# Kernel tuning notes

Measured on AMD Instinct MI355X. Metric: run time of the kernel, lower is better.

Reference implementation:

```python
import jax, jax.numpy as jnp
import numpy as np

B, S, C, D, H, FF, DEPTH, T, N = 8, 1024, 2, 512, 8, 2048, 6, 64, 16
HD = D // H
EPS = 1e-5


def _ln(x, w, b):
    m = jnp.mean(x, axis=-1, keepdims=True)
    v = jnp.mean(jnp.square(x - m), axis=-1, keepdims=True)
    return (x - m) * jax.lax.rsqrt(v + EPS) * w + b


def setup_inputs() -> dict:
    key = jax.random.key(0)
    ks = jax.random.split(key, 24)
    w = lambda k, shape: (jax.random.normal(k, shape, jnp.float32) * 0.02)
    return {
        "src": jax.random.normal(ks[0], (B, S, D), jnp.float32),
        "ctx_emb": jax.random.normal(ks[1], (B, C, D), jnp.float32),
        "times": jax.random.randint(ks[2], (B, S), 0, T),
        "spaces": jax.random.randint(ks[3], (B, S), 0, N),
        "pad_mask": jnp.zeros((B, S + C), bool),
        "time_emb": w(ks[4], (T, D)),
        "space_emb": w(ks[5], (N, D)),
        "Wqkv": w(ks[6], (DEPTH, 3 * D, D)),
        "bqkv": jnp.zeros((DEPTH, 3 * D), jnp.float32),
        "Wo": w(ks[7], (DEPTH, D, D)),
        "bo": jnp.zeros((DEPTH, D), jnp.float32),
        "ln1_w": jnp.ones((DEPTH, D), jnp.float32),
        "ln1_b": jnp.zeros((DEPTH, D), jnp.float32),
        "W1": w(ks[8], (DEPTH, FF, D)),
        "b1": jnp.zeros((DEPTH, FF), jnp.float32),
        "W2": w(ks[9], (DEPTH, D, FF)),
        "b2": jnp.zeros((DEPTH, D), jnp.float32),
        "ln2_w": jnp.ones((DEPTH, D), jnp.float32),
        "ln2_b": jnp.zeros((DEPTH, D), jnp.float32),
    }


def _forward(src, ctx_emb, times, spaces, pad_mask, time_emb, space_emb,
             Wqkv, bqkv, Wo, bo, ln1_w, ln1_b, W1, b1, W2, b2, ln2_w, ln2_b):
    NEG = -jnp.inf
    # learned time/space positional embeddings, then append context tokens
    x = src + time_emb[times] + space_emb[spaces]          # [B,S,D]
    x = jnp.concatenate([x, ctx_emb], axis=1)              # [B,L,D], L=S+C
    # per-batch additive float mask: causal-in-time over src tokens,
    # ctx tokens attendable by everyone, ctx rows attend only to ctx.
    cond = times[:, :, None] >= times[:, None, :]          # [B,S,S]
    m = jnp.where(cond, 0.0, NEG)
    m = jnp.pad(m, ((0, 0), (0, C), (0, 0)), constant_values=NEG)  # ctx rows
    m = jnp.pad(m, ((0, 0), (0, 0), (0, C)), constant_values=0.0)  # ctx cols
    m = m + jnp.where(pad_mask[:, None, :], NEG, 0.0)      # key padding
    m = m[:, None]                                         # [B,1,L,L]

    scale = 1.0 / np.sqrt(HD)
    Bc, L, _ = x.shape
    for i in range(DEPTH):
        # --- self-attention (post-norm encoder layer) ---
        qkv = x @ Wqkv[i].T + bqkv[i]                      # [B,L,3D]
        q, k, v = jnp.split(qkv, 3, axis=-1)
        split = lambda t: t.reshape(Bc, L, H, HD).transpose(0, 2, 1, 3)
        q, k, v = split(q), split(k), split(v)             # [B,H,L,HD]
        scores = jnp.einsum('bhqd,bhkd->bhqk', q, k) * scale + m
        p = jax.nn.softmax(scores, axis=-1)
        a = jnp.einsum('bhqk,bhkd->bhqd', p, v)
        a = a.transpose(0, 2, 1, 3).reshape(Bc, L, D)
        a = a @ Wo[i].T + bo[i]
        x = _ln(x + a, ln1_w[i], ln1_b[i])
        # --- feed-forward ---
        h = jax.nn.gelu(x @ W1[i].T + b1[i], approximate=False)
        h = h @ W2[i].T + b2[i]
        x = _ln(x + h, ln2_w[i], ln2_b[i])
    return x[:, :S]                                        # drop ctx tokens


def reference(src, ctx_emb, times, spaces, pad_mask, time_emb, space_emb,
              Wqkv, bqkv, Wo, bo, ln1_w, ln1_b, W1, b1, W2, b2, ln2_w, ln2_b):
    return _forward(src, ctx_emb, times, spaces, pad_mask, time_emb, space_emb,
                    Wqkv, bqkv, Wo, bo, ln1_w, ln1_b, W1, b1, W2, b2, ln2_w, ln2_b)
```

## Files before the change

### kernel.cpp

```cpp
#include <hip/hip_runtime.h>
#include <hip/hip_bf16.h>

#define BB 8
#define SS 1024
#define CC 2
#define DD 512
#define NH 8
#define FF2 2048
#define NL 6
#define LL 1026
#define HD 64
#define MROWS 8208
#define MP 8320
#define KVPAD 1152

typedef __attribute__((ext_vector_type(8))) short bf16x8;
typedef __attribute__((ext_vector_type(4))) float f32x4;

typedef __attribute__((address_space(3))) void lds_void;
typedef __attribute__((address_space(1))) void g_void;

__device__ __forceinline__ void gll16(const void* g, void* l) {
  __builtin_amdgcn_global_load_lds((const g_void*)g, (lds_void*)l, 16, 0, 0);
}

__global__ __launch_bounds__(256) void cvt_bf16_k(const float* __restrict__ in,
                                                  __hip_bfloat16* __restrict__ out) {
  int i = (blockIdx.x * 256 + threadIdx.x) * 4;
  float4 v = *(const float4*)&in[i];
  out[i + 0] = __float2bfloat16(v.x);
  out[i + 1] = __float2bfloat16(v.y);
  out[i + 2] = __float2bfloat16(v.z);
  out[i + 3] = __float2bfloat16(v.w);
}

__global__ __launch_bounds__(256) void embed_k(const float* __restrict__ src,
    const float* __restrict__ ctx, const int* __restrict__ times,
    const int* __restrict__ spaces, const float* __restrict__ te,
    const float* __restrict__ se, float* __restrict__ x,
    __hip_bfloat16* __restrict__ xb) {
  int row = blockIdx.x;
  int b = row / LL, l = row % LL;
  int c = threadIdx.x * 2;
  float y0, y1;
  if (l < SS) {
    const float* sp = src + ((size_t)(b * SS + l)) * DD + c;
    int tt = times[b * SS + l], ssp = spaces[b * SS + l];
    y0 = sp[0] + te[tt * DD + c] + se[ssp * DD + c];
    y1 = sp[1] + te[tt * DD + c + 1] + se[ssp * DD + c + 1];
  } else {
    const float* cp = ctx + ((size_t)(b * CC + (l - SS))) * DD + c;
    y0 = cp[0]; y1 = cp[1];
  }
  size_t o = (size_t)row * DD + c;
  x[o] = y0; x[o + 1] = y1;
  xb[o] = __float2bfloat16(y0); xb[o + 1] = __float2bfloat16(y1);
}

template <int EPI>
__global__ __launch_bounds__(256) void gemm_bt(const __hip_bfloat16* __restrict__ A,
    const __hip_bfloat16* __restrict__ W, const float* __restrict__ bias,
    void* __restrict__ outp, int K, int N) {
  __shared__ __hip_bfloat16 As[128 * 64];
  __shared__ __hip_bfloat16 Bs[128 * 64];
  const int tid = threadIdx.x;
  const int lane = tid & 63, wv = tid >> 6;
  const int m0 = blockIdx.x * 128, n0 = blockIdx.y * 128;
  const int wr = wv >> 1, wc = wv & 1;
  const int r0 = lane & 15, kq = lane >> 4;
  f32x4 acc[4][4] = {};
  for (int k0 = 0; k0 < K; k0 += 64) {
    __syncthreads();
#pragma unroll
    for (int c = 0; c < 4; ++c) {
      int chb = c * 256 + wv * 64;
      int ch = chb + lane;
      int row = ch >> 3, cp = ch & 7;
      gll16(A + (size_t)(m0 + row) * K + k0 + cp * 8, (char*)As + chb * 16);
      gll16(W + (size_t)(n0 + row) * K + k0 + cp * 8, (char*)Bs + chb * 16);
    }
    __syncthreads();
#pragma unroll
    for (int kk = 0; kk < 64; kk += 32) {
      bf16x8 af[4], bfr[4];
#pragma unroll
      for (int m = 0; m < 4; ++m)
        af[m] = *(const bf16x8*)&As[(wr * 64 + m * 16 + r0) * 64 + kk + kq * 8];
#pragma unroll
      for (int n = 0; n < 4; ++n)
        bfr[n] = *(const bf16x8*)&Bs[(wc * 64 + n * 16 + r0) * 64 + kk + kq * 8];
#pragma unroll
      for (int m = 0; m < 4; ++m)
#pragma unroll
        for (int n = 0; n < 4; ++n)
          acc[m][n] = __builtin_amdgcn_mfma_f32_16x16x32_bf16(af[m], bfr[n], acc[m][n], 0, 0, 0);
    }
  }
#pragma unroll
  for (int m = 0; m < 4; ++m) {
    int grow_base = m0 + wr * 64 + m * 16 + kq * 4;
#pragma unroll
    for (int n = 0; n < 4; ++n) {
      int gcol = n0 + wc * 64 + n * 16 + r0;
      float bv = bias[gcol];
#pragma unroll
      for (int j = 0; j < 4; ++j) {
        int grow = grow_base + j;
        float v = acc[m][n][j] + bv;
        if (EPI == 2) v = 0.5f * v * (1.f + erff(v * 0.70710678f));
        if (EPI == 0)
          ((float*)outp)[(size_t)grow * N + gcol] = v;
        else
          ((__hip_bfloat16*)outp)[(size_t)grow * N + gcol] = __float2bfloat16(v);
      }
    }
  }
}

__global__ __launch_bounds__(256) void vtrans_k(const __hip_bfloat16* __restrict__ qkv,
                                                __hip_bfloat16* __restrict__ vt) {
  __shared__ __hip_bfloat16 tile[64][72];
  int bh = blockIdx.y;
  int b = bh >> 3, hh = bh & 7;
  int l0 = blockIdx.x * 64;
  int t = threadIdx.x;
  int lr = t >> 2, part = t & 3;
  int l = l0 + lr;
  if (l < LL) {
    const __hip_bfloat16* p = qkv + (size_t)(b * LL + l) * 1536 + 1024 + hh * 64 + part * 16;
    *(uint4*)&tile[lr][part * 16] = *(const uint4*)p;
    *(uint4*)&tile[lr][part * 16 + 8] = *(const uint4*)(p + 8);
  } else {
    uint4 z = make_uint4(0, 0, 0, 0);
    *(uint4*)&tile[lr][part * 16] = z;
    *(uint4*)&tile[lr][part * 16 + 8] = z;
  }
  __syncthreads();
  int d = t >> 2, kp = t & 3;
  __hip_bfloat16 vals[16];
#pragma unroll
  for (int i = 0; i < 16; ++i) vals[i] = tile[kp * 16 + i][d];
  __hip_bfloat16* o = vt + ((size_t)(bh * 64 + d)) * KVPAD + l0 + kp * 16;
  *(uint4*)o = *(uint4*)&vals[0];
  *(uint4*)(o + 8) = *(uint4*)&vals[8];
}

#define TK_CTX (-2000000000)
#define TQ_CTX (-1000000000)
#define TK_INV (2000000000)

__global__ __launch_bounds__(256) void attn_k(const __hip_bfloat16* __restrict__ qkv,
    const __hip_bfloat16* __restrict__ vt, const int* __restrict__ times,
    __hip_bfloat16* __restrict__ aout) {
  __shared__ __hip_bfloat16 Kl[128 * 64];
  __shared__ __hip_bfloat16 Vl[64 * 128];
  __shared__ __hip_bfloat16 Pl[4][16 * 128];
  const int tid = threadIdx.x, lane = tid & 63, wv = tid >> 6;
  const int r0 = lane & 15, kq = lane >> 4;
  int i = blockIdx.x;
  int xcd = i & 7, slot = i >> 3;
  int bhl = slot / 17;
  int qb = slot - bhl * 17;
  int bh = xcd * 8 + bhl;
  int b = bh >> 3, hh = bh & 7;
  char* plbase = (char*)&Pl[wv][0];

  const int qbase = qb * 64 + wv * 16;
  int qr = qbase + r0;
  if (qr > LL - 1) qr = LL - 1;
  const __hip_bfloat16* qp = qkv + (size_t)(b * LL + qr) * 1536 + hh * 64;
  bf16x8 qa0 = *(const bf16x8*)(qp + kq * 8);
  bf16x8 qa1 = *(const bf16x8*)(qp + 32 + kq * 8);
  int tq[4];
#pragma unroll
  for (int j = 0; j < 4; ++j) {
    int r = qbase + kq * 4 + j;
    tq[j] = (r < SS) ? times[b * SS + r] : TQ_CTX;
  }
  float m_run[4] = {-1e30f, -1e30f, -1e30f, -1e30f};
  float l_run[4] = {0.f, 0.f, 0.f, 0.f};
  f32x4 O[4] = {};
  const float scale = 0.125f;

  for (int kc = 0; kc < 9; ++kc) {
    __syncthreads();
#pragma unroll
    for (int c = 0; c < 4; ++c) {
      int chb = c * 256 + wv * 64;
      int ch = chb + lane;
      {
        int trow = ch >> 3, cp = ch & 7;
        int krow = kc * 128 + trow;
        if (krow > LL - 1) krow = LL - 1;
        int scp = cp ^ (trow & 7);
        gll16(qkv + (size_t)(b * LL + krow) * 1536 + 512 + hh * 64 + scp * 8,
              (char*)Kl + chb * 16);
      }
      {
        int d = ch >> 4, kp = ch & 15;
        int skp = kp ^ (d & 7);
        gll16(vt + ((size_t)(bh * 64 + d)) * KVPAD + kc * 128 + skp * 8,
              (char*)Vl + chb * 16);
      }
    }
    __syncthreads();
    f32x4 s[8] = {};
#pragma unroll
    for (int n = 0; n < 8; ++n) {
      int row = n * 16 + r0;
      bf16x8 kb0 = *(const bf16x8*)&Kl[row * 64 + ((kq ^ (row & 7)) * 8)];
      bf16x8 kb1 = *(const bf16x8*)&Kl[row * 64 + (((4 + kq) ^ (row & 7)) * 8)];
      s[n] = __builtin_amdgcn_mfma_f32_16x16x32_bf16(qa0, kb0, s[n], 0, 0, 0);
      s[n] = __builtin_amdgcn_mfma_f32_16x16x32_bf16(qa1, kb1, s[n], 0, 0, 0);
    }
    int tkn[8];
#pragma unroll
    for (int n = 0; n < 8; ++n) {
      int k = kc * 128 + 16 * n + r0;
      tkn[n] = (k < SS) ? times[b * SS + k] : ((k < LL) ? TK_CTX : TK_INV);
    }
    float mch[4] = {-1e30f, -1e30f, -1e30f, -1e30f};
#pragma unroll
    for (int n = 0; n < 8; ++n)
#pragma unroll
      for (int j = 0; j < 4; ++j) {
        float sv = (tq[j] >= tkn[n]) ? s[n][j] * scale : -1e30f;
        s[n][j] = sv;
        mch[j] = fmaxf(mch[j], sv);
      }
#pragma unroll
    for (int j = 0; j < 4; ++j) {
#pragma unroll
      for (int off = 1; off < 16; off <<= 1)
        mch[j] = fmaxf(mch[j], __shfl_xor(mch[j], off, 64));
    }
    float fac[4], psum[4];
#pragma unroll
    for (int j = 0; j < 4; ++j) {
      float mn = fmaxf(m_run[j], mch[j]);
      fac[j] = __expf(m_run[j] - mn);
      m_run[j] = mn;
      psum[j] = 0.f;
    }
#pragma unroll
    for (int n = 0; n < 8; ++n)
#pragma unroll
      for (int j = 0; j < 4; ++j) {
        float p = __expf(s[n][j] - m_run[j]);
        s[n][j] = p;
        psum[j] += p;
      }
#pragma unroll
    for (int j = 0; j < 4; ++j) {
#pragma unroll
      for (int off = 1; off < 16; off <<= 1)
        psum[j] += __shfl_xor(psum[j], off, 64);
      l_run[j] = l_run[j] * fac[j] + psum[j];
    }
#pragma unroll
    for (int n = 0; n < 4; ++n)
#pragma unroll
      for (int j = 0; j < 4; ++j) O[n][j] *= fac[j];
#pragma unroll
    for (int n = 0; n < 8; ++n)
#pragma unroll
      for (int j = 0; j < 4; ++j) {
        int q = kq * 4 + j;
        int byte = ((r0 + 16 * n) * 2) ^ ((q & 7) << 4);
        *(__hip_bfloat16*)(plbase + q * 256 + byte) = __float2bfloat16(s[n][j]);
      }
#pragma unroll
    for (int c = 0; c < 4; ++c) {
      int rbyte = (c * 64 + kq * 16) ^ ((r0 & 7) << 4);
      bf16x8 pa = *(const bf16x8*)(plbase + r0 * 256 + rbyte);
#pragma unroll
      for (int n = 0; n < 4; ++n) {
        int d = n * 16 + r0;
        int chv = (c * 4 + kq) ^ (r0 & 7);
        bf16x8 vb = *(const bf16x8*)&Vl[d * 128 + chv * 8];
        O[n] = __builtin_amdgcn_mfma_f32_16x16x32_bf16(pa, vb, O[n], 0, 0, 0);
      }
    }
  }
#pragma unroll
  for (int j = 0; j < 4; ++j) {
    int orow = qbase + kq * 4 + j;
    if (orow < LL) {
      float inv = 1.f / l_run[j];
#pragma unroll
      for (int n = 0; n < 4; ++n)
        aout[(size_t)(b * LL + orow) * DD + hh * 64 + n * 16 + r0] =
            __float2bfloat16(O[n][j] * inv);
    }
  }
}

__global__ __launch_bounds__(256) void ln_fuse_k(float* __restrict__ x,
    const float* __restrict__ tmp, const float* __restrict__ w,
    const float* __restrict__ bias, __hip_bfloat16* __restrict__ xb) {
  const int row = blockIdx.x;
  const int tid = threadIdx.x;
  size_t o = (size_t)row * DD + tid * 2;
  float2 v = *(const float2*)&x[o];
  float2 t = *(const float2*)&tmp[o];
  float a0 = v.x + t.x, a1 = v.y + t.y;
  float s = a0 + a1, ss = a0 * a0 + a1 * a1;
#pragma unroll
  for (int off = 1; off < 64; off <<= 1) {
    s += __shfl_xor(s, off, 64);
    ss += __shfl_xor(ss, off, 64);
  }
  __shared__ float red[8];
  const int wv = tid >> 6, lane = tid & 63;
  if (lane == 0) { red[wv] = s; red[4 + wv] = ss; }
  __syncthreads();
  s = red[0] + red[1] + red[2] + red[3];
  ss = red[4] + red[5] + red[6] + red[7];
  float mean = s * (1.f / 512.f);
  float var = ss * (1.f / 512.f) - mean * mean;
  if (var < 0.f) var = 0.f;
  float rs = rsqrtf(var + 1e-5f);
  float w0 = w[tid * 2], w1 = w[tid * 2 + 1];
  float b0 = bias[tid * 2], b1 = bias[tid * 2 + 1];
  float y0 = (a0 - mean) * rs * w0 + b0;
  float y1 = (a1 - mean) * rs * w1 + b1;
  x[o] = y0; x[o + 1] = y1;
  xb[o] = __float2bfloat16(y0); xb[o + 1] = __float2bfloat16(y1);
}

__global__ __launch_bounds__(256) void copy_out_k(const float* __restrict__ x,
                                                  float* __restrict__ out) {
  size_t i = ((size_t)blockIdx.x * 256 + threadIdx.x) * 4;
  int b = (int)(i >> 19);
  int rem = (int)(i & 524287);
  float4 v = *(const float4*)&x[(size_t)b * LL * DD + rem];
  *(float4*)&out[i] = v;
}

extern "C" void kernel_launch(void* const* d_in, const int* in_sizes, int n_in,
                              void* d_out, int out_size, void* d_ws, size_t ws_size,
                              hipStream_t stream) {
  (void)in_sizes; (void)n_in; (void)out_size; (void)ws_size;
  const float* src    = (const float*)d_in[0];
  const float* ctx    = (const float*)d_in[1];
  const int*   times  = (const int*)d_in[2];
  const int*   spaces = (const int*)d_in[3];
  const float* te     = (const float*)d_in[5];
  const float* se     = (const float*)d_in[6];
  const float* Wqkv   = (const float*)d_in[7];
  const float* bqkv   = (const float*)d_in[8];
  const float* Wo     = (const float*)d_in[9];
  const float* bo     = (const float*)d_in[10];
  const float* ln1w   = (const float*)d_in[11];
  const float* ln1b   = (const float*)d_in[12];
  const float* W1     = (const float*)d_in[13];
  const float* b1     = (const float*)d_in[14];
  const float* W2     = (const float*)d_in[15];
  const float* b2     = (const float*)d_in[16];
  const float* ln2w   = (const float*)d_in[17];
  const float* ln2b   = (const float*)d_in[18];

  char* ws = (char*)d_ws;
  size_t off = 0;
  auto alloc = [&](size_t bytes) {
    size_t o = off;
    off += (bytes + 255) & ~(size_t)255;
    return o;
  };
  float* x            = (float*)(ws + alloc((size_t)MP * DD * 4));
  __hip_bfloat16* xb  = (__hip_bfloat16*)(ws + alloc((size_t)MP * DD * 2));
  __hip_bfloat16* qkv = (__hip_bfloat16*)(ws + alloc((size_t)MP * 3 * DD * 2));
  __hip_bfloat16* abf = (__hip_bfloat16*)(ws + alloc((size_t)MP * DD * 2));
  __hip_bfloat16* hbf = (__hip_bfloat16*)(ws + alloc((size_t)MP * FF2 * 2));
  float* tmp          = (float*)(ws + alloc((size_t)MP * DD * 4));
  __hip_bfloat16* vt  = (__hip_bfloat16*)(ws + alloc((size_t)BB * NH * HD * KVPAD * 2));
  __hip_bfloat16* wqb = (__hip_bfloat16*)(ws + alloc((size_t)NL * 3 * DD * DD * 2));
  __hip_bfloat16* wob = (__hip_bfloat16*)(ws + alloc((size_t)NL * DD * DD * 2));
  __hip_bfloat16* w1b = (__hip_bfloat16*)(ws + alloc((size_t)NL * FF2 * DD * 2));
  __hip_bfloat16* w2b = (__hip_bfloat16*)(ws + alloc((size_t)NL * DD * FF2 * 2));

  cvt_bf16_k<<<(NL * 3 * DD * DD) / 1024, 256, 0, stream>>>(Wqkv, wqb);
  cvt_bf16_k<<<(NL * DD * DD) / 1024, 256, 0, stream>>>(Wo, wob);
  cvt_bf16_k<<<(NL * FF2 * DD) / 1024, 256, 0, stream>>>(W1, w1b);
  cvt_bf16_k<<<(NL * DD * FF2) / 1024, 256, 0, stream>>>(W2, w2b);

  embed_k<<<MROWS, 256, 0, stream>>>(src, ctx, times, spaces, te, se, x, xb);

  for (int i = 0; i < NL; ++i) {
    gemm_bt<1><<<dim3(MP / 128, 12), 256, 0, stream>>>(
        xb, wqb + (size_t)i * 3 * DD * DD, bqkv + i * 3 * DD, qkv, DD, 3 * DD);
    vtrans_k<<<dim3(17, BB * NH), 256, 0, stream>>>(qkv, vt);
    attn_k<<<1088, 256, 0, stream>>>(qkv, vt, times, abf);
    gemm_bt<0><<<dim3(MP / 128, 4), 256, 0, stream>>>(
        abf, wob + (size_t)i * DD * DD, bo + i * DD, tmp, DD, DD);
    ln_fuse_k<<<MROWS, 256, 0, stream>>>(x, tmp, ln1w + i * DD, ln1b + i * DD, xb);
    gemm_bt<2><<<dim3(MP / 128, 16), 256, 0, stream>>>(
        xb, w1b + (size_t)i * FF2 * DD, b1 + i * FF2, hbf, DD, FF2);
    gemm_bt<0><<<dim3(MP / 128, 4), 256, 0, stream>>>(
        hbf, w2b + (size_t)i * DD * FF2, b2 + i * DD, tmp, FF2, DD);
    ln_fuse_k<<<MROWS, 256, 0, stream>>>(x, tmp, ln2w + i * DD, ln2b + i * DD, xb);
  }

  copy_out_k<<<(BB * SS * DD) / 1024, 256, 0, stream>>>(x, (float*)d_out);
}
```

Baseline: 1.563 ms.

## Add 128x256 GEMM tiles, XCD-aware block remap, move output bias into layernorm

Adds a 512-thread GEMM variant with 128x256 tiles for the QKV and FFN1 projections, so each loaded A tile is reused across twice as many output columns. Both GEMM kernels now use a 1D grid remapped so that consecutive tiles land on the same XCD, which should improve L2 reuse of shared A/W tiles. The bias add for the fp32-output GEMMs is dropped from the epilogue and folded into the layernorm fuse kernel. The larger tiles mean fewer blocks (390 and 520), which could lower occupancy and parallelism.

```diff
diff --git a/kernel.cpp b/kernel.cpp
--- a/kernel.cpp
+++ b/kernel.cpp
@@ -65,7 +65,12 @@
   __shared__ __hip_bfloat16 Bs[128 * 64];
   const int tid = threadIdx.x;
   const int lane = tid & 63, wv = tid >> 6;
-  const int m0 = blockIdx.x * 128, n0 = blockIdx.y * 128;
+  const int ny = N >> 7;
+  const int nwg = gridDim.x;
+  int qq = nwg >> 3, rr = nwg & 7;
+  int xcd = blockIdx.x & 7, loc = blockIdx.x >> 3;
+  int slot = (xcd < rr ? xcd * (qq + 1) : rr * (qq + 1) + (xcd - rr) * qq) + loc;
+  const int m0 = (slot / ny) * 128, n0 = (slot % ny) * 128;
   const int wr = wv >> 1, wc = wv & 1;
   const int r0 = lane & 15, kq = lane >> 4;
   f32x4 acc[4][4] = {};
@@ -102,7 +107,76 @@
 #pragma unroll
     for (int n = 0; n < 4; ++n) {
       int gcol = n0 + wc * 64 + n * 16 + r0;
-      float bv = bias[gcol];
+      float bv = (EPI == 0) ? 0.f : bias[gcol];
+#pragma unroll
+      for (int j = 0; j < 4; ++j) {
+        int grow = grow_base + j;
+        float v = acc[m][n][j] + bv;
+        if (EPI == 2) v = 0.5f * v * (1.f + erff(v * 0.70710678f));
+        if (EPI == 0)
+          ((float*)outp)[(size_t)grow * N + gcol] = v;
+        else
+          ((__hip_bfloat16*)outp)[(size_t)grow * N + gcol] = __float2bfloat16(v);
+      }
+    }
+  }
+}
+
+template <int EPI>
+__global__ __launch_bounds__(512) void gemm_bt2(const __hip_bfloat16* __restrict__ A,
+    const __hip_bfloat16* __restrict__ W, const float* __restrict__ bias,
+    void* __restrict__ outp, int K, int N) {
+  __shared__ __hip_bfloat16 As[128 * 64];
+  __shared__ __hip_bfloat16 Bs[256 * 64];
+  const int tid = threadIdx.x;
+  const int lane = tid & 63, wv = tid >> 6;
+  const int ny = N >> 8;
+  const int nwg = gridDim.x;
+  int qq = nwg >> 3, rr = nwg & 7;
+  int xcd = blockIdx.x & 7, loc = blockIdx.x >> 3;
+  int slot = (xcd < rr ? xcd * (qq + 1) : rr * (qq + 1) + (xcd - rr) * qq) + loc;
+  const int m0 = (slot / ny) * 128, n0 = (slot % ny) * 256;
+  const int wr = wv >> 2, wc = wv & 3;
+  const int r0 = lane & 15, kq = lane >> 4;
+  f32x4 acc[4][4] = {};
+  for (int k0 = 0; k0 < K; k0 += 64) {
+    __syncthreads();
+#pragma unroll
+    for (int c = 0; c < 6; ++c) {
+      int ch = c * 512 + tid;
+      if (ch < 1024) {
+        int row = ch >> 3, cp = ch & 7;
+        gll16(A + (size_t)(m0 + row) * K + k0 + cp * 8, (char*)As + ch * 16);
+      } else {
+        int bi = ch - 1024;
+        int row = bi >> 3, cp = bi & 7;
+        gll16(W + (size_t)(n0 + row) * K + k0 + cp * 8, (char*)Bs + bi * 16);
+      }
+    }
+    __syncthreads();
+#pragma unroll
+    for (int kk = 0; kk < 64; kk += 32) {
+      bf16x8 af[4], bfr[4];
+#pragma unroll
+      for (int m = 0; m < 4; ++m)
+        af[m] = *(const bf16x8*)&As[(wr * 64 + m * 16 + r0) * 64 + kk + kq * 8];
+#pragma unroll
+      for (int n = 0; n < 4; ++n)
+        bfr[n] = *(const bf16x8*)&Bs[(wc * 64 + n * 16 + r0) * 64 + kk + kq * 8];
+#pragma unroll
+      for (int m = 0; m < 4; ++m)
+#pragma unroll
+        for (int n = 0; n < 4; ++n)
+          acc[m][n] = __builtin_amdgcn_mfma_f32_16x16x32_bf16(af[m], bfr[n], acc[m][n], 0, 0, 0);
+    }
+  }
+#pragma unroll
+  for (int m = 0; m < 4; ++m) {
+    int grow_base = m0 + wr * 64 + m * 16 + kq * 4;
+#pragma unroll
+    for (int n = 0; n < 4; ++n) {
+      int gcol = n0 + wc * 64 + n * 16 + r0;
+      float bv = (EPI == 0) ? 0.f : bias[gcol];
 #pragma unroll
       for (int j = 0; j < 4; ++j) {
         int grow = grow_base + j;
@@ -296,14 +370,15 @@
 }
 
 __global__ __launch_bounds__(256) void ln_fuse_k(float* __restrict__ x,
-    const float* __restrict__ tmp, const float* __restrict__ w,
-    const float* __restrict__ bias, __hip_bfloat16* __restrict__ xb) {
+    const float* __restrict__ tmp, const float* __restrict__ gb,
+    const float* __restrict__ w, const float* __restrict__ bias,
+    __hip_bfloat16* __restrict__ xb) {
   const int row = blockIdx.x;
   const int tid = threadIdx.x;
   size_t o = (size_t)row * DD + tid * 2;
   float2 v = *(const float2*)&x[o];
   float2 t = *(const float2*)&tmp[o];
-  float a0 = v.x + t.x, a1 = v.y + t.y;
+  float a0 = v.x + gb[tid * 2] + t.x, a1 = v.y + gb[tid * 2 + 1] + t.y;
   float s = a0 + a1, ss = a0 * a0 + a1 * a1;
 #pragma unroll
   for (int off = 1; off < 64; off <<= 1) {
@@ -387,18 +462,20 @@
   embed_k<<<MROWS, 256, 0, stream>>>(src, ctx, times, spaces, te, se, x, xb);
 
   for (int i = 0; i < NL; ++i) {
-    gemm_bt<1><<<dim3(MP / 128, 12), 256, 0, stream>>>(
+    gemm_bt2<1><<<65 * 6, 512, 0, stream>>>(
         xb, wqb + (size_t)i * 3 * DD * DD, bqkv + i * 3 * DD, qkv, DD, 3 * DD);
     vtrans_k<<<dim3(17, BB * NH), 256, 0, stream>>>(qkv, vt);
     attn_k<<<1088, 256, 0, stream>>>(qkv, vt, times, abf);
-    gemm_bt<0><<<dim3(MP / 128, 4), 256, 0, stream>>>(
-        abf, wob + (size_t)i * DD * DD, bo + i * DD, tmp, DD, DD);
-    ln_fuse_k<<<MROWS, 256, 0, stream>>>(x, tmp, ln1w + i * DD, ln1b + i * DD, xb);
-    gemm_bt<2><<<dim3(MP / 128, 16), 256, 0, stream>>>(
+    gemm_bt<0><<<65 * 4, 256, 0, stream>>>(
+        abf, wob + (size_t)i * DD * DD, nullptr, tmp, DD, DD);
+    ln_fuse_k<<<MROWS, 256, 0, stream>>>(x, tmp, bo + i * DD,
+                                         ln1w + i * DD, ln1b + i * DD, xb);
+    gemm_bt2<2><<<65 * 8, 512, 0, stream>>>(
         xb, w1b + (size_t)i * FF2 * DD, b1 + i * FF2, hbf, DD, FF2);
-    gemm_bt<0><<<dim3(MP / 128, 4), 256, 0, stream>>>(
-        hbf, w2b + (size_t)i * DD * FF2, b2 + i * DD, tmp, FF2, DD);
-    ln_fuse_k<<<MROWS, 256, 0, stream>>>(x, tmp, ln2w + i * DD, ln2b + i * DD, xb);
+    gemm_bt<0><<<65 * 4, 256, 0, stream>>>(
+        hbf, w2b + (size_t)i * DD * FF2, nullptr, tmp, FF2, DD);
+    ln_fuse_k<<<MROWS, 256, 0, stream>>>(x, tmp, b2 + i * DD,
+                                         ln2w + i * DD, ln2b + i * DD, xb);
   }
 
   copy_out_k<<<(BB * SS * DD) / 1024, 256, 0, stream>>>(x, (float*)d_out);
```

After: 1.505 ms. 1.04x faster.
